# Performance work log

Hardware: AMD Instinct MI355X
Metric: run time of the kernel (lower is better)

Reference implementation:

```python
import jax, jax.numpy as jnp
import numpy as np

N, E = 4096, 131072
IN, HID, OUT = 128, 128, 256
H4, C4 = 4, HID            # first/middle GAT: 4 heads of 128 -> concat 512
CAT = H4 * C4              # 512
NH, DK = 8, OUT // 8       # dense MHA
EPS_LN = 1e-5


def setup_inputs() -> dict:
    key = jax.random.key(0)
    ks = jax.random.split(key, 32)
    s = 0.05
    inp = {
        "x": jax.random.normal(ks[0], (N, IN), jnp.float32),
        "edge_index": jax.random.randint(ks[1], (2, E), 0, N, jnp.int64),
        # GAT layer 0: in=128, heads=4, out=128
        "W0": jax.random.normal(ks[2], (IN, H4 * C4)) * s,
        "as0": jax.random.normal(ks[3], (H4, C4)) * s,
        "ad0": jax.random.normal(ks[4], (H4, C4)) * s,
        "b0": jnp.zeros((H4 * C4,)),
        # GAT layer 1: in=512, heads=4, out=128
        "W1": jax.random.normal(ks[5], (CAT, H4 * C4)) * s,
        "as1": jax.random.normal(ks[6], (H4, C4)) * s,
        "ad1": jax.random.normal(ks[7], (H4, C4)) * s,
        "b1": jnp.zeros((H4 * C4,)),
        # GAT layer 2: in=512, heads=1, out=256
        "W2": jax.random.normal(ks[8], (CAT, OUT)) * s,
        "as2": jax.random.normal(ks[9], (1, OUT)) * s,
        "ad2": jax.random.normal(ks[10], (1, OUT)) * s,
        "b2": jnp.zeros((OUT,)),
        # LayerNorms
        "g0": jnp.ones((CAT,)), "be0": jnp.zeros((CAT,)),
        "g1": jnp.ones((CAT,)), "be1": jnp.zeros((CAT,)),
        "g2": jnp.ones((OUT,)), "be2": jnp.zeros((OUT,)),
        # dense MHA on output_dim=256
        "wq": jax.random.normal(ks[11], (OUT, OUT)) * s, "bq": jnp.zeros((OUT,)),
        "wk": jax.random.normal(ks[12], (OUT, OUT)) * s, "bk": jnp.zeros((OUT,)),
        "wv": jax.random.normal(ks[13], (OUT, OUT)) * s, "bv": jnp.zeros((OUT,)),
        "wo": jax.random.normal(ks[14], (OUT, OUT)) * s, "bo": jnp.zeros((OUT,)),
    }
    return inp


def _layer_norm(x, g, b):
    mu = x.mean(-1, keepdims=True)
    var = ((x - mu) ** 2).mean(-1, keepdims=True)
    return (x - mu) * jax.lax.rsqrt(var + EPS_LN) * g + b


def _gat(x, src, dst, W, a_src, a_dst, bias, heads, out_c):
    # PyG GATConv (concat=True, negative_slope=0.2, self-loops pre-added)
    n = x.shape[0]
    xl = (x @ W).reshape(n, heads, out_c)            # [N,H,C]
    al_s = (xl * a_src).sum(-1)                      # [N,H]
    al_d = (xl * a_dst).sum(-1)                      # [N,H]
    alpha = jax.nn.leaky_relu(al_s[src] + al_d[dst], 0.2)  # [Etot,H]
    m = jax.ops.segment_max(alpha, dst, num_segments=n)
    e = jnp.exp(alpha - m[dst])
    denom = jax.ops.segment_sum(e, dst, num_segments=n)
    w = e / (denom[dst] + 1e-16)                     # [Etot,H]
    msg = w[:, :, None] * xl[src]                    # [Etot,H,C]
    out = jax.ops.segment_sum(msg, dst, num_segments=n)
    return out.reshape(n, heads * out_c) + bias


def _mha(x, wq, bq, wk, bk, wv, bv, wo, bo):
    # x: [1,N,D], 8 heads
    B, S, D = x.shape
    def split(y):
        return y.reshape(B, S, NH, DK).transpose(0, 2, 1, 3)
    Q, K, V = split(x @ wq + bq), split(x @ wk + bk), split(x @ wv + bv)
    scores = jnp.einsum('bhqd,bhkd->bhqk', Q, K) / np.sqrt(DK)
    attn = jax.nn.softmax(scores, axis=-1)
    out = jnp.einsum('bhqk,bhkd->bhqd', attn, V)
    out = out.transpose(0, 2, 1, 3).reshape(B, S, D)
    return out @ wo + bo


def reference(x, edge_index, W0, as0, ad0, b0, W1, as1, ad1, b1, W2, as2, ad2, b2,
              g0, be0, g1, be1, g2, be2, wq, bq, wk, bk, wv, bv, wo, bo):
    n = x.shape[0]
    loops = jnp.arange(n, dtype=edge_index.dtype)
    src = jnp.concatenate([edge_index[0], loops])
    dst = jnp.concatenate([edge_index[1], loops])

    # layer 0: in=128 -> 512; residual None (128 != 512)
    h = jax.nn.elu(_gat(x, src, dst, W0, as0, ad0, b0, H4, C4))
    h = _layer_norm(h, g0, be0)

    # layer 1: 512 -> 512; residual applies
    res = h
    h = jax.nn.elu(_gat(h, src, dst, W1, as1, ad1, b1, H4, C4))
    h = _layer_norm(h, g1, be1)
    h = h + res

    # layer 2: 512 -> 256, 1 head
    h = _gat(h, src, dst, W2, as2, ad2, b2, 1, OUT)
    h = _layer_norm(h, g2, be2)

    # dense self-attention over all nodes as one sequence
    h = _mha(h[None], wq, bq, wk, bk, wv, bv, wo, bo)[0]
    return h
```

## Files before the change

### kernel.cpp

```cpp
#include <hip/hip_runtime.h>
#include <math.h>

typedef __attribute__((ext_vector_type(8))) short short8;
typedef __attribute__((ext_vector_type(4))) float float4v;

#define QS 0.2550354f

#if __has_builtin(__builtin_amdgcn_exp2f)
#define EXP2(x) __builtin_amdgcn_exp2f(x)
#else
#define EXP2(x) __expf((x)*0.6931471805599453f)
#endif

__device__ __forceinline__ float waveReduceSum(float v){
  #pragma unroll
  for(int o=32;o>0;o>>=1) v += __shfl_down(v,o,64);
  return v;
}

__device__ __forceinline__ unsigned short f2bf(float f){
  unsigned int u = __float_as_uint(f);
  return (unsigned short)((u + 0x7FFFu + ((u>>16)&1u)) >> 16);
}
__device__ __forceinline__ float bf2f(unsigned short u){
  return __uint_as_float(((unsigned int)u)<<16);
}

__global__ __launch_bounds__(256) void prep(const float* __restrict__ x, unsigned short* __restrict__ xb,
                     const float* __restrict__ W0, unsigned short* __restrict__ W0t,
                     const float* __restrict__ W1, unsigned short* __restrict__ W1t,
                     const float* __restrict__ W2, unsigned short* __restrict__ W2t,
                     const float* __restrict__ wq, const float* __restrict__ wk,
                     const float* __restrict__ wv, unsigned short* __restrict__ wqkvt,
                     const float* __restrict__ bq, const float* __restrict__ bk,
                     const float* __restrict__ bv, float* __restrict__ bqkv,
                     const float* __restrict__ wo, unsigned short* __restrict__ wot,
                     const float* __restrict__ as0, const float* __restrict__ ad0, unsigned short* __restrict__ S0,
                     const float* __restrict__ as1, const float* __restrict__ ad1, unsigned short* __restrict__ S1,
                     const float* __restrict__ as2, const float* __restrict__ ad2, unsigned short* __restrict__ S2,
                     const int* __restrict__ ei, int E, int Etot, int* __restrict__ hist){
  int b = blockIdx.x, t = threadIdx.x;
  if(b < 256){
    int i = (b*256 + t)*8;
    float4 u0 = *(const float4*)(x + i);
    float4 u1 = *(const float4*)(x + i + 4);
    short8 o;
    o[0]=(short)f2bf(u0.x); o[1]=(short)f2bf(u0.y); o[2]=(short)f2bf(u0.z); o[3]=(short)f2bf(u0.w);
    o[4]=(short)f2bf(u1.x); o[5]=(short)f2bf(u1.y); o[6]=(short)f2bf(u1.z); o[7]=(short)f2bf(u1.w);
    *(short8*)(xb + i) = o;
    return;
  }
  if(b == 256){ bqkv[t] = bq[t]*QS; bqkv[256+t] = bk[t]; bqkv[512+t] = bv[t]; return; }
  if(b < 433){
    __shared__ unsigned short tile[64][65];
    int tb = b - 257;
    const float* src; unsigned short* dst; int K,N,roff,local; float sc = 1.f;
    if(tb<16){src=W0;dst=W0t;K=128;N=512;local=tb;roff=0;}
    else if(tb<80){src=W1;dst=W1t;K=512;N=512;local=tb-16;roff=0;}
    else if(tb<112){src=W2;dst=W2t;K=512;N=256;local=tb-80;roff=0;}
    else if(tb<128){src=wq;dst=wqkvt;K=256;N=256;local=tb-112;roff=0;sc=QS;}
    else if(tb<144){src=wk;dst=wqkvt;K=256;N=256;local=tb-128;roff=256;}
    else if(tb<160){src=wv;dst=wqkvt;K=256;N=256;local=tb-144;roff=512;}
    else {src=wo;dst=wot;K=256;N=256;local=tb-160;roff=0;}
    int ntiles = N>>6;
    int k0 = (local/ntiles)*64, n0 = (local%ntiles)*64;
    int r4 = t>>4, c4 = (t&15)*4;
    #pragma unroll
    for(int it=0;it<4;it++){
      int row = r4 + it*16;
      float4 v = *(const float4*)(src + (size_t)(k0+row)*N + n0 + c4);
      tile[row][c4+0]=f2bf(v.x*sc);
      tile[row][c4+1]=f2bf(v.y*sc);
      tile[row][c4+2]=f2bf(v.z*sc);
      tile[row][c4+3]=f2bf(v.w*sc);
    }
    __syncthreads();
    int r8 = t>>3, c8 = (t&7)*8;
    #pragma unroll
    for(int it=0;it<2;it++){
      int n = r8 + it*32;
      short8 o;
      #pragma unroll
      for(int j=0;j<8;j++) o[j] = (short)tile[c8+j][n];
      *(short8*)(dst + (size_t)(n0+n+roff)*K + k0 + c8) = o;
    }
    return;
  }
  if(b >= 1585){
    int e = (b-1585)*256 + t;
    if(e < Etot){
      int d = (e<E) ? (ei[E+e]&4095) : (e-E);
      atomicAdd(&hist[d], 1);
    }
    return;
  }
  int bb = b - 433;
  const float *W,*as,*ad; unsigned short* S; int K,C,H,k;
  if(bb<128){W=W0;as=as0;ad=ad0;S=S0;K=128;C=128;H=4;k=bb;}
  else if(bb<640){W=W1;as=as1;ad=ad1;S=S1;K=512;C=128;H=4;k=bb-128;}
  else {W=W2;as=as2;ad=ad2;S=S2;K=512;C=256;H=1;k=bb-640;}
  int D = H*C;
  __shared__ float s1[4], s2[4];
  int lane=t&63, wid=t>>6;
  for(int h=0;h<H;h++){
    float ps=0.f, pd=0.f;
    for(int c=t;c<C;c+=256){
      float wv2 = W[k*D + h*C + c];
      ps += wv2*as[h*C+c];
      pd += wv2*ad[h*C+c];
    }
    ps = waveReduceSum(ps); pd = waveReduceSum(pd);
    if(lane==0){ s1[wid]=ps; s2[wid]=pd; }
    __syncthreads();
    if(t==0){
      float u=s1[0]+s1[1]+s1[2]+s1[3], v=s2[0]+s2[1]+s2[2]+s2[3];
      S[h*K+k]=f2bf(u); S[(4+h)*K+k]=f2bf(v);
    }
    __syncthreads();
  }
  if(t==0){
    for(int h=H;h<4;h++){ S[h*K+k]=0; S[(4+h)*K+k]=0; }
    for(int r=8;r<16;r++) S[r*K+k]=0;
  }
}

__global__ __launch_bounds__(256) void gemm_mfma(const unsigned short* __restrict__ A,
                                                 const unsigned short* __restrict__ Bt,
                                                 const float* __restrict__ bias,
                                                 float* __restrict__ C,
                                                 unsigned short* __restrict__ Cb,
                                                 unsigned short* __restrict__ VtT,
                                                 const unsigned short* __restrict__ Wsd,
                                                 float* __restrict__ als,
                                                 float* __restrict__ ald,
                                                 int M, int K, int N){
  int t = threadIdx.x, lane = t & 63, w = t >> 6;
  int m = lane & 15, g = lane >> 4;
  int bm = blockIdx.y * 64, bn = blockIdx.x * 64;

  __shared__ unsigned short As[2][64*72];
  __shared__ unsigned short Bs[2][64*72];

  int sr = t >> 3;
  int sc = (t & 7) * 8;
  const unsigned short* Ap = A  + (bm + sr)*K + sc;
  const unsigned short* Bp = Bt + (bn + sr)*K + sc;
  bool doC = (Wsd != nullptr) && (blockIdx.x == 0);

  float4v acc[4];
  #pragma unroll
  for(int nt=0;nt<4;nt++) acc[nt] = (float4v){0.f,0.f,0.f,0.f};
  float4v acc2 = (float4v){0.f,0.f,0.f,0.f};

  short8 a0 = *(const short8*)(Ap);
  short8 a1 = *(const short8*)(Ap + 32*K);
  short8 b0 = *(const short8*)(Bp);
  short8 b1 = *(const short8*)(Bp + 32*K);

  int buf = 0;
  for(int k0=0;k0<K;k0+=64){
    *(short8*)&As[buf][sr*72 + sc]      = a0;
    *(short8*)&As[buf][(sr+32)*72 + sc] = a1;
    *(short8*)&Bs[buf][sr*72 + sc]      = b0;
    *(short8*)&Bs[buf][(sr+32)*72 + sc] = b1;
    if(k0+64 < K){
      a0 = *(const short8*)(Ap + k0+64);
      a1 = *(const short8*)(Ap + 32*K + k0+64);
      b0 = *(const short8*)(Bp + k0+64);
      b1 = *(const short8*)(Bp + 32*K + k0+64);
    }
    __syncthreads();

    #pragma unroll
    for(int ks=0;ks<2;ks++){
      short8 aA = *(const short8*)&As[buf][(w*16 + m)*72 + ks*32 + g*8];
      #pragma unroll
      for(int nt=0;nt<4;nt++){
        short8 bB = *(const short8*)&Bs[buf][(nt*16 + m)*72 + ks*32 + g*8];
        acc[nt] = __builtin_amdgcn_mfma_f32_16x16x32_bf16(aA, bB, acc[nt], 0,0,0);
      }
      if(doC){
        short8 bW = *(const short8*)(Wsd + m*K + k0 + ks*32 + g*8);
        acc2 = __builtin_amdgcn_mfma_f32_16x16x32_bf16(aA, bW, acc2, 0,0,0);
      }
    }
    buf ^= 1;
  }

  if(VtT && bn >= 512){
    __syncthreads();
    unsigned short* T = &As[0][0];
    #pragma unroll
    for(int nt=0;nt<4;nt++){
      int col = bn + nt*16 + m;
      float bv = bias ? bias[col] : 0.f;
      unsigned int r0 = __float_as_uint(acc[nt][0]+bv) + 0x8000u;
      unsigned int r1 = __float_as_uint(acc[nt][1]+bv) + 0x8000u;
      unsigned int r2 = __float_as_uint(acc[nt][2]+bv) + 0x8000u;
      unsigned int r3 = __float_as_uint(acc[nt][3]+bv) + 0x8000u;
      uint2 pk;
      pk.x = __builtin_amdgcn_perm(r1, r0, 0x07060302u);
      pk.y = __builtin_amdgcn_perm(r3, r2, 0x07060302u);
      *(uint2*)&T[(nt*16 + m)*72 + w*16 + g*4] = pk;
    }
    __syncthreads();
    int d  = t >> 2;
    int qc = (t & 3) * 16;
    short8 v0 = *(const short8*)&T[d*72 + qc];
    short8 v1 = *(const short8*)&T[d*72 + qc + 8];
    unsigned short* dst = VtT + (size_t)(bn - 512 + d)*M + bm + qc;
    *(short8*)(dst)     = v0;
    *(short8*)(dst + 8) = v1;
    return;
  }

  #pragma unroll
  for(int nt=0;nt<4;nt++){
    int col = bn + nt*16 + m;
    float bv = bias ? bias[col] : 0.f;
    #pragma unroll
    for(int r=0;r<4;r++){
      int row = bm + w*16 + g*4 + r;
      float v = acc[nt][r] + bv;
      if(C)  C[row*N + col]  = v;
      if(Cb) Cb[row*N + col] = f2bf(v);
    }
  }
  if(doC){
    #pragma unroll
    for(int r=0;r<4;r++){
      int row = bm + w*16 + g*4 + r;
      if(m<4)      als[row*4 + m]     = acc2[r];
      else if(m<8) ald[row*4 + (m-4)] = acc2[r];
    }
  }
}

__global__ __launch_bounds__(1024) void csr_scan(const int* __restrict__ hist,
                                                 int* __restrict__ row_ptr,
                                                 int* __restrict__ wcnt, int N){
  __shared__ int sh[1024];
  int t = threadIdx.x;
  int base[4];
  int s = 0;
  #pragma unroll
  for(int i=0;i<4;i++){ base[i]=s; s += hist[t*4+i]; }
  sh[t] = s;
  __syncthreads();
  for(int off=1; off<1024; off<<=1){
    int x = (t>=off) ? sh[t-off] : 0;
    __syncthreads();
    sh[t] += x;
    __syncthreads();
  }
  int excl = (t==0) ? 0 : sh[t-1];
  #pragma unroll
  for(int i=0;i<4;i++){
    row_ptr[t*4+i] = excl + base[i];
    wcnt[t*4+i]    = excl + base[i];
  }
  if(t==1023) row_ptr[N] = excl + s;
}

__global__ void csr_scatter(const int* __restrict__ ei, int E, int Etot,
                            int* __restrict__ wcnt, int* __restrict__ col){
  int e = blockIdx.x*256 + threadIdx.x;
  if(e>=Etot) return;
  int s,d;
  if(e<E){ s=ei[e]&4095; d=ei[E+e]&4095; } else { s=d=e-E; }
  int pos = atomicAdd(&wcnt[d], 1);
  col[pos] = s;
}

#define CE 128
__global__ void gat_gather_ln(const int* __restrict__ rp,
                              const int* __restrict__ col,
                              const unsigned short* __restrict__ xlb,
                              const float* __restrict__ als,
                              const float* __restrict__ ald,
                              const float* __restrict__ bias,
                              const float* __restrict__ gw,
                              const float* __restrict__ be,
                              const float* __restrict__ res,
                              float* __restrict__ out,
                              unsigned short* __restrict__ outb,
                              int D, int logC, int do_elu){
  int n = blockIdx.x, t = threadIdx.x;
  int c0 = t*2;
  int h = c0 >> logC;
  int rowW = D >> 1;
  float4 advv = *(const float4*)(ald + n*4);
  int start = rp[n], end = rp[n+1];
  const unsigned int* xw = (const unsigned int*)xlb;

  __shared__ float pw[2][CE*4];
  __shared__ int offs[2][CE];

  float acc0=0.f, acc1=0.f, den=0.f;
  int nch = (end - start + CE - 1) / CE;

  {
    int cnt = min(CE, end-start);
    if(t < cnt){
      int s = col[start+t];
      offs[0][t] = s*rowW;
      float4 av = *(const float4*)(als + s*4);
      #pragma unroll
      for(int hh=0;hh<4;hh++){
        float a = ((const float*)&av)[hh] + ((const float*)&advv)[hh];
        a = a>0.f ? a : 0.2f*a;
        pw[0][t*4+hh] = __expf(a);
      }
    }
  }

  for(int c=0;c<nch;c++){
    __syncthreads();
    if(c+1 < nch){
      int base = start + (c+1)*CE;
      int cnt = min(CE, end-base);
      int b2 = (c+1)&1;
      if(t < cnt){
        int s = col[base+t];
        offs[b2][t] = s*rowW;
        float4 av = *(const float4*)(als + s*4);
        #pragma unroll
        for(int hh=0;hh<4;hh++){
          float a = ((const float*)&av)[hh] + ((const float*)&advv)[hh];
          a = a>0.f ? a : 0.2f*a;
          pw[b2][t*4+hh] = __expf(a);
        }
      }
    }
    int base = start + c*CE;
    int cnt = min(CE, end-base);
    int b = c&1;
    #pragma unroll 8
    for(int j=0;j<cnt;j++){
      float p = pw[b][j*4+h];
      unsigned int u = xw[offs[b][j] + t];
      acc0 += p * bf2f((unsigned short)(u & 0xffffu));
      acc1 += p * bf2f((unsigned short)(u >> 16));
      den += p;
    }
  }

  float inv_d = 1.f/(den + 1e-16f);
  float v0 = acc0*inv_d + bias[c0];
  float v1 = acc1*inv_d + bias[c0+1];
  if(do_elu){
    v0 = v0>0.f ? v0 : expm1f(v0);
    v1 = v1>0.f ? v1 : expm1f(v1);
  }
  __shared__ float sh[4];
  int lane=t&63, wid=t>>6, nw = blockDim.x>>6;
  float sum = waveReduceSum(v0+v1);
  if(lane==0) sh[wid]=sum;
  __syncthreads();
  float mean = 0.f;
  for(int i=0;i<nw;i++) mean += sh[i];
  mean /= (float)D;
  __syncthreads();
  float d0 = v0-mean, d1 = v1-mean;
  float vs = waveReduceSum(d0*d0 + d1*d1);
  if(lane==0) sh[wid]=vs;
  __syncthreads();
  float var = 0.f;
  for(int i=0;i<nw;i++) var += sh[i];
  var /= (float)D;
  float inv = rsqrtf(var + 1e-5f);
  float y0 = d0*inv*gw[c0]   + be[c0];
  float y1 = d1*inv*gw[c0+1] + be[c0+1];
  if(res){ float2 rv = *(const float2*)(res + n*D + c0); y0 += rv.x; y1 += rv.y; }
  if(out) *(float2*)(out + n*D + c0) = make_float2(y0, y1);
  if(outb) ((unsigned int*)outb)[n*rowW + t] =
      (unsigned int)f2bf(y0) | ((unsigned int)f2bf(y1) << 16);
}

#define KS 4
__global__ __launch_bounds__(256) void attention12(const unsigned short* __restrict__ QKV,
                                                   const unsigned short* __restrict__ Vt,
                                                   float* __restrict__ Op,
                                                   float* __restrict__ lp, int S){
  const int RS = 768;
  int qb = blockIdx.x * 64;
  int h  = blockIdx.y;
  int ks = blockIdx.z;
  int t  = threadIdx.x;
  int lane = t & 63, w = t >> 6;
  int m = lane & 15, g = lane >> 4;
  int m7 = m & 7;

  __shared__ unsigned short Ps[64*64];
  __shared__ unsigned short Vs[32*64];
  __shared__ unsigned short Ks[64*36];

  short8 aQ = *(const short8*)(QKV + (qb + w*16 + m)*RS + h*32 + g*8);

  float4v o0 = {0.f,0.f,0.f,0.f}, o1 = {0.f,0.f,0.f,0.f};
  float den = 0.f;

  int r8 = t>>3, c8 = t&7;
  int kr = t>>2, kc = (t&3)*8;
  int kA = ks*(S/KS), kB = kA + S/KS;

  short8 v  = *(const short8*)(Vt + (h*32 + r8)*S + kA + c8*8);
  short8 kv = *(const short8*)(QKV + (kA + kr)*RS + 256 + h*32 + kc);

  for(int kt=kA; kt<kB; kt+=64){
    __syncthreads();
    *(short8*)&Vs[r8*64 + ((c8 ^ (r8&7))<<3)] = v;
    *(short8*)&Ks[kr*36 + kc] = kv;
    if(kt+64 < kB){
      v  = *(const short8*)(Vt + (h*32 + r8)*S + kt+64 + c8*8);
      kv = *(const short8*)(QKV + (kt+64 + kr)*RS + 256 + h*32 + kc);
    }
    __syncthreads();

    #pragma unroll
    for(int nt=0;nt<4;nt++){
      short8 aK = *(const short8*)&Ks[(nt*16 + m)*36 + g*8];
      float4v acc = {0.f,0.f,0.f,0.f};
      acc = __builtin_amdgcn_mfma_f32_16x16x32_bf16(aK, aQ, acc, 0,0,0);
      float p0 = EXP2(acc[0]);
      float p1 = EXP2(acc[1]);
      float p2 = EXP2(acc[2]);
      float p3 = EXP2(acc[3]);
      den += (p0+p1)+(p2+p3);
      unsigned int r0 = __float_as_uint(p0) + 0x8000u;
      unsigned int r1 = __float_as_uint(p1) + 0x8000u;
      unsigned int r2 = __float_as_uint(p2) + 0x8000u;
      unsigned int r3 = __float_as_uint(p3) + 0x8000u;
      uint2 pk;
      pk.x = __builtin_amdgcn_perm(r1, r0, 0x07060302u);
      pk.y = __builtin_amdgcn_perm(r3, r2, 0x07060302u);
      *(uint2*)&Ps[(w*16 + m)*64 + (((2*nt + (g>>1)) ^ m7)<<3) + ((g&1)<<2)] = pk;
    }

    #pragma unroll
    for(int kh=0;kh<2;kh++){
      int swz = ((kh*4 + g) ^ m7) << 3;
      short8 aP  = *(const short8*)&Ps[(w*16 + m)*64 + swz];
      short8 bV0 = *(const short8*)&Vs[m*64       + swz];
      short8 bV1 = *(const short8*)&Vs[(16+m)*64  + swz];
      o0 = __builtin_amdgcn_mfma_f32_16x16x32_bf16(aP, bV0, o0, 0,0,0);
      o1 = __builtin_amdgcn_mfma_f32_16x16x32_bf16(aP, bV1, o1, 0,0,0);
    }
  }

  den += __shfl_xor(den, 16, 64);
  den += __shfl_xor(den, 32, 64);

  float* Ob = Op + (size_t)ks*S*256;
  #pragma unroll
  for(int r=0;r<4;r++){
    int q = qb + w*16 + g*4 + r;
    Ob[q*256 + h*32 + m]      = o0[r];
    Ob[q*256 + h*32 + 16 + m] = o1[r];
  }
  if(g==0){
    int q = qb + w*16 + m;
    lp[ks*S*8 + q*8 + h] = den;
  }
}

__global__ __launch_bounds__(256) void combine(const float* __restrict__ Op,
                                               const float* __restrict__ lp,
                                               unsigned short* __restrict__ aob, int S){
  int q = blockIdx.x, t = threadIdx.x;
  int h = t >> 5;
  float o = 0.f, l = 0.f;
  #pragma unroll
  for(int s=0;s<KS;s++) o += Op[(size_t)s*S*256 + q*256 + t];
  #pragma unroll
  for(int s=0;s<KS;s++) l += lp[s*S*8 + q*8 + h];
  aob[q*256 + t] = f2bf(o / l);
}

extern "C" void kernel_launch(void* const* d_in, const int* in_sizes, int n_in,
                              void* d_out, int out_size, void* d_ws, size_t ws_size,
                              hipStream_t stream) {
  const float* x   = (const float*)d_in[0];
  const int*   ei  = (const int*)d_in[1];
  const float* W0  = (const float*)d_in[2];
  const float* as0 = (const float*)d_in[3];
  const float* ad0 = (const float*)d_in[4];
  const float* b0  = (const float*)d_in[5];
  const float* W1  = (const float*)d_in[6];
  const float* as1 = (const float*)d_in[7];
  const float* ad1 = (const float*)d_in[8];
  const float* b1  = (const float*)d_in[9];
  const float* W2  = (const float*)d_in[10];
  const float* as2 = (const float*)d_in[11];
  const float* ad2 = (const float*)d_in[12];
  const float* b2  = (const float*)d_in[13];
  const float* g0  = (const float*)d_in[14];
  const float* be0 = (const float*)d_in[15];
  const float* g1  = (const float*)d_in[16];
  const float* be1 = (const float*)d_in[17];
  const float* g2  = (const float*)d_in[18];
  const float* be2 = (const float*)d_in[19];
  const float* wq  = (const float*)d_in[20];
  const float* bq  = (const float*)d_in[21];
  const float* wk  = (const float*)d_in[22];
  const float* bk  = (const float*)d_in[23];
  const float* wv  = (const float*)d_in[24];
  const float* bv  = (const float*)d_in[25];
  const float* wo  = (const float*)d_in[26];
  const float* bo  = (const float*)d_in[27];
  float* out = (float*)d_out;

  const int N = 4096;
  const int E = in_sizes[1] / 2;
  const int Etot = E + N;

  char* p = (char*)d_ws;
  auto alloc = [&](size_t bytes){ char* r = p; p += (bytes + 255) & ~(size_t)255; return r; };

  float* h0   = (float*)alloc(N*512*4);
  float* als  = (float*)alloc(N*4*4);
  float* ald  = (float*)alloc(N*4*4);
  unsigned short* xb   = (unsigned short*)alloc(N*128*2);
  unsigned short* xlb  = (unsigned short*)alloc(N*512*2);
  unsigned short* h0b  = (unsigned short*)alloc(N*512*2);
  unsigned short* h1b  = (unsigned short*)alloc(N*512*2);
  unsigned short* h2b  = (unsigned short*)alloc(N*256*2);
  unsigned short* QKVb = (unsigned short*)alloc((size_t)N*768*2);
  unsigned short* Vt   = (unsigned short*)alloc(256*N*2);
  unsigned short* aob  = (unsigned short*)alloc(N*256*2);
  unsigned short* W0t  = (unsigned short*)alloc(512*128*2);
  unsigned short* W1t  = (unsigned short*)alloc(512*512*2);
  unsigned short* W2t  = (unsigned short*)alloc(256*512*2);
  unsigned short* wqkvt= (unsigned short*)alloc(768*256*2);
  float* bqkv = (float*)alloc(768*4);
  unsigned short* wot  = (unsigned short*)alloc(256*256*2);
  unsigned short* Wsd0 = (unsigned short*)alloc(16*128*2);
  unsigned short* Wsd1 = (unsigned short*)alloc(16*512*2);
  unsigned short* Wsd2 = (unsigned short*)alloc(16*512*2);
  float* Op = (float*)alloc((size_t)KS*N*256*4);
  float* lp = (float*)alloc((size_t)KS*N*8*4);
  int* hist = (int*)alloc(N*4);
  int* wcnt = (int*)alloc(N*4);
  int* rp   = (int*)alloc((N+2)*4);
  int* col  = (int*)alloc(Etot*4);

  hipMemsetAsync(hist, 0, N*sizeof(int), stream);
  prep<<<1585 + (Etot+255)/256, 256, 0, stream>>>(x, xb, W0, W0t, W1, W1t, W2, W2t,
                                 wq, wk, wv, wqkvt, bq, bk, bv, bqkv, wo, wot,
                                 as0, ad0, Wsd0, as1, ad1, Wsd1, as2, ad2, Wsd2,
                                 ei, E, Etot, hist);

  csr_scan<<<1, 1024, 0, stream>>>(hist, rp, wcnt, N);
  csr_scatter<<<(Etot+255)/256, 256, 0, stream>>>(ei, E, Etot, wcnt, col);

  gemm_mfma<<<dim3(8, 64), 256, 0, stream>>>(xb, W0t, nullptr, nullptr, xlb, nullptr, Wsd0, als, ald, N, 128, 512);
  gat_gather_ln<<<N, 256, 0, stream>>>(rp, col, xlb, als, ald, b0, g0, be0,
                                       nullptr, h0, h0b, 512, 7, 1);

  gemm_mfma<<<dim3(8, 64), 256, 0, stream>>>(h0b, W1t, nullptr, nullptr, xlb, nullptr, Wsd1, als, ald, N, 512, 512);
  gat_gather_ln<<<N, 256, 0, stream>>>(rp, col, xlb, als, ald, b1, g1, be1,
                                       h0, nullptr, h1b, 512, 7, 1);

  gemm_mfma<<<dim3(4, 64), 256, 0, stream>>>(h1b, W2t, nullptr, nullptr, xlb, nullptr, Wsd2, als, ald, N, 512, 256);
  gat_gather_ln<<<N, 128, 0, stream>>>(rp, col, xlb, als, ald, b2, g2, be2,
                                       nullptr, nullptr, h2b, 256, 8, 0);

  gemm_mfma<<<dim3(12, 64), 256, 0, stream>>>(h2b, wqkvt, bqkv, nullptr, QKVb, Vt, nullptr, nullptr, nullptr, N, 256, 768);
  attention12<<<dim3(N/64, 8, KS), 256, 0, stream>>>(QKVb, Vt, Op, lp, N);
  combine<<<N, 256, 0, stream>>>(Op, lp, aob, N);
  gemm_mfma<<<dim3(4, 64), 256, 0, stream>>>(aob, wot, bo, out, nullptr, nullptr, nullptr, nullptr, nullptr, N, 256, 256);
}
```

Before: 268.1 us.

## Fuse whole pipeline into one cooperative persistent kernel with grid syncs

Replaces the sequence of separate launches (prep, CSR scan/scatter, GEMMs, GAT gathers, attention, combine, output GEMM) with a single cooperative megakernel of 512 persistent blocks that loop over work units and separate stages with grid.sync(). It aims to remove per-launch overhead and the inter-kernel gaps between about fourteen small kernels. The attention path appears restructured into a per-block unit writing aob directly, dropping the split-K partial buffers and combine pass. In exchange, each stage is limited to 512 blocks with shared-memory reuse, occupancy is capped, and grid-wide barriers add their own latency.

Result: slower. 1.029 ms (+283.9%).

```diff
diff --git a/kernel.cpp b/kernel.cpp
--- a/kernel.cpp
+++ b/kernel.cpp
@@ -1,10 +1,14 @@
 #include <hip/hip_runtime.h>
+#include <hip/hip_cooperative_groups.h>
 #include <math.h>
+
+namespace cg = cooperative_groups;
 
 typedef __attribute__((ext_vector_type(8))) short short8;
 typedef __attribute__((ext_vector_type(4))) float float4v;
 
 #define QS 0.2550354f
+#define NB 512
 
 #if __has_builtin(__builtin_amdgcn_exp2f)
 #define EXP2(x) __builtin_amdgcn_exp2f(x)
@@ -17,7 +21,6 @@
   for(int o=32;o>0;o>>=1) v += __shfl_down(v,o,64);
   return v;
 }
-
 __device__ __forceinline__ unsigned short f2bf(float f){
   unsigned int u = __float_as_uint(f);
   return (unsigned short)((u + 0x7FFFu + ((u>>16)&1u)) >> 16);
@@ -26,81 +29,65 @@
   return __uint_as_float(((unsigned int)u)<<16);
 }
 
-__global__ __launch_bounds__(256) void prep(const float* __restrict__ x, unsigned short* __restrict__ xb,
-                     const float* __restrict__ W0, unsigned short* __restrict__ W0t,
-                     const float* __restrict__ W1, unsigned short* __restrict__ W1t,
-                     const float* __restrict__ W2, unsigned short* __restrict__ W2t,
-                     const float* __restrict__ wq, const float* __restrict__ wk,
-                     const float* __restrict__ wv, unsigned short* __restrict__ wqkvt,
-                     const float* __restrict__ bq, const float* __restrict__ bk,
-                     const float* __restrict__ bv, float* __restrict__ bqkv,
-                     const float* __restrict__ wo, unsigned short* __restrict__ wot,
-                     const float* __restrict__ as0, const float* __restrict__ ad0, unsigned short* __restrict__ S0,
-                     const float* __restrict__ as1, const float* __restrict__ ad1, unsigned short* __restrict__ S1,
-                     const float* __restrict__ as2, const float* __restrict__ ad2, unsigned short* __restrict__ S2,
-                     const int* __restrict__ ei, int E, int Etot, int* __restrict__ hist){
-  int b = blockIdx.x, t = threadIdx.x;
-  if(b < 256){
-    int i = (b*256 + t)*8;
-    float4 u0 = *(const float4*)(x + i);
-    float4 u1 = *(const float4*)(x + i + 4);
+struct MP {
+  const float* x; const int* ei;
+  const float *W0,*as0,*ad0,*b0;
+  const float *W1,*as1,*ad1,*b1;
+  const float *W2,*as2,*ad2,*b2;
+  const float *g0,*be0,*g1,*be1,*g2,*be2;
+  const float *wq,*bq,*wk,*bk,*wv,*bv,*wo,*bo;
+  float* out;
+  float *h0,*als,*ald,*bqkv;
+  unsigned short *xb,*xlb,*h0b,*h1b,*h2b,*QKVb,*Vt,*aob;
+  unsigned short *W0t,*W1t,*W2t,*wqkvt,*wot,*Wsd0,*Wsd1,*Wsd2;
+  int *hist,*wcnt,*rp,*col;
+  int E, Etot;
+};
+
+
+__device__ void transpose_unit(int tb, const MP& P, char* smem){
+  int t = threadIdx.x;
+  unsigned short (*tile)[65] = (unsigned short(*)[65])smem;
+  const float* src; unsigned short* dst; int K,N,roff,local; float sc = 1.f;
+  if(tb<16){src=P.W0;dst=P.W0t;K=128;N=512;local=tb;roff=0;}
+  else if(tb<80){src=P.W1;dst=P.W1t;K=512;N=512;local=tb-16;roff=0;}
+  else if(tb<112){src=P.W2;dst=P.W2t;K=512;N=256;local=tb-80;roff=0;}
+  else if(tb<128){src=P.wq;dst=P.wqkvt;K=256;N=256;local=tb-112;roff=0;sc=QS;}
+  else if(tb<144){src=P.wk;dst=P.wqkvt;K=256;N=256;local=tb-128;roff=256;}
+  else if(tb<160){src=P.wv;dst=P.wqkvt;K=256;N=256;local=tb-144;roff=512;}
+  else {src=P.wo;dst=P.wot;K=256;N=256;local=tb-160;roff=0;}
+  int ntiles = N>>6;
+  int k0 = (local/ntiles)*64, n0 = (local%ntiles)*64;
+  int r4 = t>>4, c4 = (t&15)*4;
+  #pragma unroll
+  for(int it=0;it<4;it++){
+    int row = r4 + it*16;
+    float4 v = *(const float4*)(src + (size_t)(k0+row)*N + n0 + c4);
+    tile[row][c4+0]=f2bf(v.x*sc);
+    tile[row][c4+1]=f2bf(v.y*sc);
+    tile[row][c4+2]=f2bf(v.z*sc);
+    tile[row][c4+3]=f2bf(v.w*sc);
+  }
+  __syncthreads();
+  int r8 = t>>3, c8 = (t&7)*8;
+  #pragma unroll
+  for(int it=0;it<2;it++){
+    int n = r8 + it*32;
     short8 o;
-    o[0]=(short)f2bf(u0.x); o[1]=(short)f2bf(u0.y); o[2]=(short)f2bf(u0.z); o[3]=(short)f2bf(u0.w);
-    o[4]=(short)f2bf(u1.x); o[5]=(short)f2bf(u1.y); o[6]=(short)f2bf(u1.z); o[7]=(short)f2bf(u1.w);
-    *(short8*)(xb + i) = o;
-    return;
-  }
-  if(b == 256){ bqkv[t] = bq[t]*QS; bqkv[256+t] = bk[t]; bqkv[512+t] = bv[t]; return; }
-  if(b < 433){
-    __shared__ unsigned short tile[64][65];
-    int tb = b - 257;
-    const float* src; unsigned short* dst; int K,N,roff,local; float sc = 1.f;
-    if(tb<16){src=W0;dst=W0t;K=128;N=512;local=tb;roff=0;}
-    else if(tb<80){src=W1;dst=W1t;K=512;N=512;local=tb-16;roff=0;}
-    else if(tb<112){src=W2;dst=W2t;K=512;N=256;local=tb-80;roff=0;}
-    else if(tb<128){src=wq;dst=wqkvt;K=256;N=256;local=tb-112;roff=0;sc=QS;}
-    else if(tb<144){src=wk;dst=wqkvt;K=256;N=256;local=tb-128;roff=256;}
-    else if(tb<160){src=wv;dst=wqkvt;K=256;N=256;local=tb-144;roff=512;}
-    else {src=wo;dst=wot;K=256;N=256;local=tb-160;roff=0;}
-    int ntiles = N>>6;
-    int k0 = (local/ntiles)*64, n0 = (local%ntiles)*64;
-    int r4 = t>>4, c4 = (t&15)*4;
     #pragma unroll
-    for(int it=0;it<4;it++){
-      int row = r4 + it*16;
-      float4 v = *(const float4*)(src + (size_t)(k0+row)*N + n0 + c4);
-      tile[row][c4+0]=f2bf(v.x*sc);
-      tile[row][c4+1]=f2bf(v.y*sc);
-      tile[row][c4+2]=f2bf(v.z*sc);
-      tile[row][c4+3]=f2bf(v.w*sc);
-    }
-    __syncthreads();
-    int r8 = t>>3, c8 = (t&7)*8;
-    #pragma unroll
-    for(int it=0;it<2;it++){
-      int n = r8 + it*32;
-      short8 o;
-      #pragma unroll
-      for(int j=0;j<8;j++) o[j] = (short)tile[c8+j][n];
-      *(short8*)(dst + (size_t)(n0+n+roff)*K + k0 + c8) = o;
-    }
-    return;
-  }
-  if(b >= 1585){
-    int e = (b-1585)*256 + t;
-    if(e < Etot){
-      int d = (e<E) ? (ei[E+e]&4095) : (e-E);
-      atomicAdd(&hist[d], 1);
-    }
-    return;
-  }
-  int bb = b - 433;
+    for(int j=0;j<8;j++) o[j] = (short)tile[c8+j][n];
+    *(short8*)(dst + (size_t)(n0+n+roff)*K + k0 + c8) = o;
+  }
+}
+
+__device__ void wsd_unit(int bb, const MP& P, char* smem){
+  int t = threadIdx.x;
+  float* s1 = (float*)smem; float* s2 = s1+4;
   const float *W,*as,*ad; unsigned short* S; int K,C,H,k;
-  if(bb<128){W=W0;as=as0;ad=ad0;S=S0;K=128;C=128;H=4;k=bb;}
-  else if(bb<640){W=W1;as=as1;ad=ad1;S=S1;K=512;C=128;H=4;k=bb-128;}
-  else {W=W2;as=as2;ad=ad2;S=S2;K=512;C=256;H=1;k=bb-640;}
+  if(bb<128){W=P.W0;as=P.as0;ad=P.ad0;S=P.Wsd0;K=128;C=128;H=4;k=bb;}
+  else if(bb<640){W=P.W1;as=P.as1;ad=P.ad1;S=P.Wsd1;K=512;C=128;H=4;k=bb-128;}
+  else {W=P.W2;as=P.as2;ad=P.ad2;S=P.Wsd2;K=512;C=256;H=1;k=bb-640;}
   int D = H*C;
-  __shared__ float s1[4], s2[4];
   int lane=t&63, wid=t>>6;
   for(int h=0;h<H;h++){
     float ps=0.f, pd=0.f;
@@ -124,28 +111,48 @@
   }
 }
 
-__global__ __launch_bounds__(256) void gemm_mfma(const unsigned short* __restrict__ A,
-                                                 const unsigned short* __restrict__ Bt,
-                                                 const float* __restrict__ bias,
-                                                 float* __restrict__ C,
-                                                 unsigned short* __restrict__ Cb,
-                                                 unsigned short* __restrict__ VtT,
-                                                 const unsigned short* __restrict__ Wsd,
-                                                 float* __restrict__ als,
-                                                 float* __restrict__ ald,
-                                                 int M, int K, int N){
+__device__ void scan_block(const int* __restrict__ hist, int* __restrict__ rp,
+                           int* __restrict__ wcnt, char* smem){
+  int t = threadIdx.x;
+  int* sh = (int*)smem;
+  int loc[16]; int s=0;
+  #pragma unroll
+  for(int i=0;i<16;i++){ loc[i]=s; s += hist[t*16+i]; }
+  sh[t] = s;
+  __syncthreads();
+  for(int off=1; off<256; off<<=1){
+    int x = (t>=off) ? sh[t-off] : 0;
+    __syncthreads();
+    sh[t] += x;
+    __syncthreads();
+  }
+  int excl = (t==0) ? 0 : sh[t-1];
+  #pragma unroll
+  for(int i=0;i<16;i++){
+    int v = excl + loc[i];
+    rp[t*16+i] = v; wcnt[t*16+i] = v;
+  }
+  if(t==255) rp[4096] = excl + s;
+}
+
+__device__ void gemm_unit(int u, int nbx,
+                          const unsigned short* __restrict__ A, const unsigned short* __restrict__ Bt,
+                          const float* __restrict__ bias, float* __restrict__ C,
+                          unsigned short* __restrict__ Cb, unsigned short* __restrict__ VtT,
+                          const unsigned short* __restrict__ Wsd, float* __restrict__ als,
+                          float* __restrict__ ald, int M, int K, int N, char* smem){
   int t = threadIdx.x, lane = t & 63, w = t >> 6;
   int m = lane & 15, g = lane >> 4;
-  int bm = blockIdx.y * 64, bn = blockIdx.x * 64;
-
-  __shared__ unsigned short As[2][64*72];
-  __shared__ unsigned short Bs[2][64*72];
+  int bx = u % nbx, by = u / nbx;
+  int bm = by * 64, bn = bx * 64;
+  unsigned short* As = (unsigned short*)smem;
+  unsigned short* Bs = (unsigned short*)(smem + 18432);
 
   int sr = t >> 3;
   int sc = (t & 7) * 8;
-  const unsigned short* Ap = A  + (bm + sr)*K + sc;
-  const unsigned short* Bp = Bt + (bn + sr)*K + sc;
-  bool doC = (Wsd != nullptr) && (blockIdx.x == 0);
+  const unsigned short* Ap = A  + (size_t)(bm + sr)*K + sc;
+  const unsigned short* Bp = Bt + (size_t)(bn + sr)*K + sc;
+  bool doC = (Wsd != nullptr) && (bx == 0);
 
   float4v acc[4];
   #pragma unroll
@@ -159,10 +166,10 @@
 
   int buf = 0;
   for(int k0=0;k0<K;k0+=64){
-    *(short8*)&As[buf][sr*72 + sc]      = a0;
-    *(short8*)&As[buf][(sr+32)*72 + sc] = a1;
-    *(short8*)&Bs[buf][sr*72 + sc]      = b0;
-    *(short8*)&Bs[buf][(sr+32)*72 + sc] = b1;
+    *(short8*)&As[buf*4608 + sr*72 + sc]      = a0;
+    *(short8*)&As[buf*4608 + (sr+32)*72 + sc] = a1;
+    *(short8*)&Bs[buf*4608 + sr*72 + sc]      = b0;
+    *(short8*)&Bs[buf*4608 + (sr+32)*72 + sc] = b1;
     if(k0+64 < K){
       a0 = *(const short8*)(Ap + k0+64);
       a1 = *(const short8*)(Ap + 32*K + k0+64);
@@ -173,10 +180,10 @@
 
     #pragma unroll
     for(int ks=0;ks<2;ks++){
-      short8 aA = *(const short8*)&As[buf][(w*16 + m)*72 + ks*32 + g*8];
+      short8 aA = *(const short8*)&As[buf*4608 + (w*16 + m)*72 + ks*32 + g*8];
       #pragma unroll
       for(int nt=0;nt<4;nt++){
-        short8 bB = *(const short8*)&Bs[buf][(nt*16 + m)*72 + ks*32 + g*8];
+        short8 bB = *(const short8*)&Bs[buf*4608 + (nt*16 + m)*72 + ks*32 + g*8];
         acc[nt] = __builtin_amdgcn_mfma_f32_16x16x32_bf16(aA, bB, acc[nt], 0,0,0);
       }
       if(doC){
@@ -187,9 +194,9 @@
     buf ^= 1;
   }
 
-  if(VtT && bn >= 512){
-    __syncthreads();
-    unsigned short* T = &As[0][0];
+  if(VtT != nullptr && bn >= 512){
+    __syncthreads();
+    unsigned short* T = As;
     #pragma unroll
     for(int nt=0;nt<4;nt++){
       int col = bn + nt*16 + m;
@@ -211,90 +218,50 @@
     unsigned short* dst = VtT + (size_t)(bn - 512 + d)*M + bm + qc;
     *(short8*)(dst)     = v0;
     *(short8*)(dst + 8) = v1;
-    return;
-  }
-
-  #pragma unroll
-  for(int nt=0;nt<4;nt++){
-    int col = bn + nt*16 + m;
-    float bv = bias ? bias[col] : 0.f;
+  } else {
     #pragma unroll
-    for(int r=0;r<4;r++){
-      int row = bm + w*16 + g*4 + r;
-      float v = acc[nt][r] + bv;
-      if(C)  C[row*N + col]  = v;
-      if(Cb) Cb[row*N + col] = f2bf(v);
-    }
-  }
-  if(doC){
-    #pragma unroll
-    for(int r=0;r<4;r++){
-      int row = bm + w*16 + g*4 + r;
-      if(m<4)      als[row*4 + m]     = acc2[r];
-      else if(m<8) ald[row*4 + (m-4)] = acc2[r];
-    }
-  }
-}
-
-__global__ __launch_bounds__(1024) void csr_scan(const int* __restrict__ hist,
-                                                 int* __restrict__ row_ptr,
-                                                 int* __restrict__ wcnt, int N){
-  __shared__ int sh[1024];
+    for(int nt=0;nt<4;nt++){
+      int col = bn + nt*16 + m;
+      float bv = bias ? bias[col] : 0.f;
+      #pragma unroll
+      for(int r=0;r<4;r++){
+        int row = bm + w*16 + g*4 + r;
+        float v = acc[nt][r] + bv;
+        if(C)  C[(size_t)row*N + col]  = v;
+        if(Cb) Cb[(size_t)row*N + col] = f2bf(v);
+      }
+    }
+    if(doC){
+      #pragma unroll
+      for(int r=0;r<4;r++){
+        int row = bm + w*16 + g*4 + r;
+        if(m<4)      als[row*4 + m]     = acc2[r];
+        else if(m<8) ald[row*4 + (m-4)] = acc2[r];
+      }
+    }
+  }
+  __syncthreads();
+}
+
+#define CE 128
+__device__ void gat_node(int n, const int* __restrict__ rp, const int* __restrict__ col,
+                         const unsigned short* __restrict__ xlb,
+                         const float* __restrict__ als, const float* __restrict__ ald,
+                         const float* __restrict__ bias, const float* __restrict__ gw,
+                         const float* __restrict__ be, const float* __restrict__ res,
+                         float* __restrict__ out, unsigned short* __restrict__ outb,
+                         int D, int logC, int do_elu, int nw, char* smem){
   int t = threadIdx.x;
-  int base[4];
-  int s = 0;
-  #pragma unroll
-  for(int i=0;i<4;i++){ base[i]=s; s += hist[t*4+i]; }
-  sh[t] = s;
-  __syncthreads();
-  for(int off=1; off<1024; off<<=1){
-    int x = (t>=off) ? sh[t-off] : 0;
-    __syncthreads();
-    sh[t] += x;
-    __syncthreads();
-  }
-  int excl = (t==0) ? 0 : sh[t-1];
-  #pragma unroll
-  for(int i=0;i<4;i++){
-    row_ptr[t*4+i] = excl + base[i];
-    wcnt[t*4+i]    = excl + base[i];
-  }
-  if(t==1023) row_ptr[N] = excl + s;
-}
-
-__global__ void csr_scatter(const int* __restrict__ ei, int E, int Etot,
-                            int* __restrict__ wcnt, int* __restrict__ col){
-  int e = blockIdx.x*256 + threadIdx.x;
-  if(e>=Etot) return;
-  int s,d;
-  if(e<E){ s=ei[e]&4095; d=ei[E+e]&4095; } else { s=d=e-E; }
-  int pos = atomicAdd(&wcnt[d], 1);
-  col[pos] = s;
-}
-
-#define CE 128
-__global__ void gat_gather_ln(const int* __restrict__ rp,
-                              const int* __restrict__ col,
-                              const unsigned short* __restrict__ xlb,
-                              const float* __restrict__ als,
-                              const float* __restrict__ ald,
-                              const float* __restrict__ bias,
-                              const float* __restrict__ gw,
-                              const float* __restrict__ be,
-                              const float* __restrict__ res,
-                              float* __restrict__ out,
-                              unsigned short* __restrict__ outb,
-                              int D, int logC, int do_elu){
-  int n = blockIdx.x, t = threadIdx.x;
+  float* pw  = (float*)smem;
+  int*  offs = (int*)(smem + 4096);
+  float* shv = (float*)(smem + 4096 + 1024);
+  int halfD = D >> 1;
+  bool act = t < halfD;
   int c0 = t*2;
   int h = c0 >> logC;
-  int rowW = D >> 1;
   float4 advv = *(const float4*)(ald + n*4);
   int start = rp[n], end = rp[n+1];
   const unsigned int* xw = (const unsigned int*)xlb;
-
-  __shared__ float pw[2][CE*4];
-  __shared__ int offs[2][CE];
 
   float acc0=0.f, acc1=0.f, den=0.f;
   int nch = (end - start + CE - 1) / CE;
@@ -303,13 +270,13 @@
     int cnt = min(CE, end-start);
     if(t < cnt){
       int s = col[start+t];
-      offs[0][t] = s*rowW;
+      offs[t] = s*halfD;
       float4 av = *(const float4*)(als + s*4);
       #pragma unroll
       for(int hh=0;hh<4;hh++){
         float a = ((const float*)&av)[hh] + ((const float*)&advv)[hh];
         a = a>0.f ? a : 0.2f*a;
-        pw[0][t*4+hh] = __expf(a);
+        pw[t*4+hh] = __expf(a);
       }
     }
   }
@@ -317,18 +284,18 @@
   for(int c=0;c<nch;c++){
     __syncthreads();
     if(c+1 < nch){
-      int base = start + (c+1)*CE;
-      int cnt = min(CE, end-base);
+      int base2 = start + (c+1)*CE;
+      int cnt = min(CE, end-base2);
       int b2 = (c+1)&1;
       if(t < cnt){
-        int s = col[base+t];
-        offs[b2][t] = s*rowW;
+        int s = col[base2+t];
+        offs[b2*CE+t] = s*halfD;
         float4 av = *(const float4*)(als + s*4);
         #pragma unroll
         for(int hh=0;hh<4;hh++){
           float a = ((const float*)&av)[hh] + ((const float*)&advv)[hh];
           a = a>0.f ? a : 0.2f*a;
-          pw[b2][t*4+hh] = __expf(a);
+          pw[b2*CE*4 + t*4+hh] = __expf(a);
         }
       }
     }
@@ -337,83 +304,84 @@
     int b = c&1;
     #pragma unroll 8
     for(int j=0;j<cnt;j++){
-      float p = pw[b][j*4+h];
-      unsigned int u = xw[offs[b][j] + t];
+      float p = pw[b*CE*4 + j*4+h];
+      unsigned int u = xw[offs[b*CE+j] + t];
       acc0 += p * bf2f((unsigned short)(u & 0xffffu));
       acc1 += p * bf2f((unsigned short)(u >> 16));
       den += p;
     }
   }
 
-  float inv_d = 1.f/(den + 1e-16f);
-  float v0 = acc0*inv_d + bias[c0];
-  float v1 = acc1*inv_d + bias[c0+1];
-  if(do_elu){
-    v0 = v0>0.f ? v0 : expm1f(v0);
-    v1 = v1>0.f ? v1 : expm1f(v1);
-  }
-  __shared__ float sh[4];
-  int lane=t&63, wid=t>>6, nw = blockDim.x>>6;
+  float v0=0.f, v1=0.f;
+  if(act){
+    float inv_d = 1.f/(den + 1e-16f);
+    v0 = acc0*inv_d + bias[c0];
+    v1 = acc1*inv_d + bias[c0+1];
+    if(do_elu){
+      v0 = v0>0.f ? v0 : expm1f(v0);
+      v1 = v1>0.f ? v1 : expm1f(v1);
+    }
+  }
+  int lane=t&63, wid=t>>6;
   float sum = waveReduceSum(v0+v1);
-  if(lane==0) sh[wid]=sum;
+  if(lane==0) shv[wid]=sum;
   __syncthreads();
   float mean = 0.f;
-  for(int i=0;i<nw;i++) mean += sh[i];
+  for(int i=0;i<nw;i++) mean += shv[i];
   mean /= (float)D;
   __syncthreads();
-  float d0 = v0-mean, d1 = v1-mean;
+  float d0 = act ? v0-mean : 0.f;
+  float d1 = act ? v1-mean : 0.f;
   float vs = waveReduceSum(d0*d0 + d1*d1);
-  if(lane==0) sh[wid]=vs;
+  if(lane==0) shv[wid]=vs;
   __syncthreads();
   float var = 0.f;
-  for(int i=0;i<nw;i++) var += sh[i];
+  for(int i=0;i<nw;i++) var += shv[i];
   var /= (float)D;
   float inv = rsqrtf(var + 1e-5f);
-  float y0 = d0*inv*gw[c0]   + be[c0];
-  float y1 = d1*inv*gw[c0+1] + be[c0+1];
-  if(res){ float2 rv = *(const float2*)(res + n*D + c0); y0 += rv.x; y1 += rv.y; }
-  if(out) *(float2*)(out + n*D + c0) = make_float2(y0, y1);
-  if(outb) ((unsigned int*)outb)[n*rowW + t] =
-      (unsigned int)f2bf(y0) | ((unsigned int)f2bf(y1) << 16);
-}
-
-#define KS 4
-__global__ __launch_bounds__(256) void attention12(const unsigned short* __restrict__ QKV,
-                                                   const unsigned short* __restrict__ Vt,
-                                                   float* __restrict__ Op,
-                                                   float* __restrict__ lp, int S){
+  if(act){
+    float y0 = d0*inv*gw[c0]   + be[c0];
+    float y1 = d1*inv*gw[c0+1] + be[c0+1];
+    if(res){ float2 rv = *(const float2*)(res + (size_t)n*D + c0); y0 += rv.x; y1 += rv.y; }
+    if(out) *(float2*)(out + (size_t)n*D + c0) = make_float2(y0, y1);
+    if(outb) ((unsigned int*)outb)[(size_t)n*halfD + t] =
+        (unsigned int)f2bf(y0) | ((unsigned int)f2bf(y1) << 16);
+  }
+}
+
+__device__ void attn_unit(int u, const unsigned short* __restrict__ QKV,
+                          const unsigned short* __restrict__ Vt,
+                          unsigned short* __restrict__ aob, int S, char* smem){
   const int RS = 768;
-  int qb = blockIdx.x * 64;
-  int h  = blockIdx.y;
-  int ks = blockIdx.z;
+  int qb = (u >> 3) * 64;
+  int h  = u & 7;
   int t  = threadIdx.x;
   int lane = t & 63, w = t >> 6;
   int m = lane & 15, g = lane >> 4;
   int m7 = m & 7;
 
-  __shared__ unsigned short Ps[64*64];
-  __shared__ unsigned short Vs[32*64];
-  __shared__ unsigned short Ks[64*36];
-
-  short8 aQ = *(const short8*)(QKV + (qb + w*16 + m)*RS + h*32 + g*8);
+  unsigned short* Ps = (unsigned short*)smem;
+  unsigned short* Vs = (unsigned short*)(smem + 8192);
+  unsigned short* Ks = (unsigned short*)(smem + 12288);
+
+  short8 aQ = *(const short8*)(QKV + (size_t)(qb + w*16 + m)*RS + h*32 + g*8);
 
   float4v o0 = {0.f,0.f,0.f,0.f}, o1 = {0.f,0.f,0.f,0.f};
   float den = 0.f;
 
   int r8 = t>>3, c8 = t&7;
   int kr = t>>2, kc = (t&3)*8;
-  int kA = ks*(S/KS), kB = kA + S/KS;
-
-  short8 v  = *(const short8*)(Vt + (h*32 + r8)*S + kA + c8*8);
-  short8 kv = *(const short8*)(QKV + (kA + kr)*RS + 256 + h*32 + kc);
-
-  for(int kt=kA; kt<kB; kt+=64){
+
+  short8 v  = *(const short8*)(Vt + (size_t)(h*32 + r8)*S + c8*8);
+  short8 kv = *(const short8*)(QKV + (size_t)kr*RS + 256 + h*32 + kc);
+
+  for(int kt=0; kt<S; kt+=64){
     __syncthreads();
     *(short8*)&Vs[r8*64 + ((c8 ^ (r8&7))<<3)] = v;
     *(short8*)&Ks[kr*36 + kc] = kv;
-    if(kt+64 < kB){
-      v  = *(const short8*)(Vt + (h*32 + r8)*S + kt+64 + c8*8);
-      kv = *(const short8*)(QKV + (kt+64 + kr)*RS + 256 + h*32 + kc);
+    if(kt+64 < S){
+      v  = *(const short8*)(Vt + (size_t)(h*32 + r8)*S + kt+64 + c8*8);
+      kv = *(const short8*)(QKV + (size_t)(kt+64 + kr)*RS + 256 + h*32 + kc);
     }
     __syncthreads();
 
@@ -451,65 +419,111 @@
   den += __shfl_xor(den, 16, 64);
   den += __shfl_xor(den, 32, 64);
 
-  float* Ob = Op + (size_t)ks*S*256;
   #pragma unroll
   for(int r=0;r<4;r++){
+    float dd = __shfl(den, g*4 + r, 64);
     int q = qb + w*16 + g*4 + r;
-    Ob[q*256 + h*32 + m]      = o0[r];
-    Ob[q*256 + h*32 + 16 + m] = o1[r];
-  }
-  if(g==0){
-    int q = qb + w*16 + m;
-    lp[ks*S*8 + q*8 + h] = den;
-  }
-}
-
-__global__ __launch_bounds__(256) void combine(const float* __restrict__ Op,
-                                               const float* __restrict__ lp,
-                                               unsigned short* __restrict__ aob, int S){
-  int q = blockIdx.x, t = threadIdx.x;
-  int h = t >> 5;
-  float o = 0.f, l = 0.f;
-  #pragma unroll
-  for(int s=0;s<KS;s++) o += Op[(size_t)s*S*256 + q*256 + t];
-  #pragma unroll
-  for(int s=0;s<KS;s++) l += lp[s*S*8 + q*8 + h];
-  aob[q*256 + t] = f2bf(o / l);
+    aob[(size_t)q*256 + h*32 + m]      = f2bf(o0[r]/dd);
+    aob[(size_t)q*256 + h*32 + 16 + m] = f2bf(o1[r]/dd);
+  }
+}
+
+__global__ __launch_bounds__(256, 2) void mega(MP P){
+  __shared__ __attribute__((aligned(16))) char smem[36880];
+  cg::grid_group grid = cg::this_grid();
+  int blk = blockIdx.x, t = threadIdx.x;
+
+  { int gid = blk*256 + t; if(gid < 4096) P.hist[gid] = 0; }
+  for(int u=blk; u<1585; u+=NB){
+    if(u < 256){
+      int i = (u*256 + t)*8;
+      float4 u0 = *(const float4*)(P.x + i);
+      float4 u1 = *(const float4*)(P.x + i + 4);
+      short8 o;
+      o[0]=(short)f2bf(u0.x); o[1]=(short)f2bf(u0.y); o[2]=(short)f2bf(u0.z); o[3]=(short)f2bf(u0.w);
+      o[4]=(short)f2bf(u1.x); o[5]=(short)f2bf(u1.y); o[6]=(short)f2bf(u1.z); o[7]=(short)f2bf(u1.w);
+      *(short8*)(P.xb + i) = o;
+    } else if(u == 256){
+      P.bqkv[t] = P.bq[t]*QS; P.bqkv[256+t] = P.bk[t]; P.bqkv[512+t] = P.bv[t];
+    } else if(u < 433){
+      transpose_unit(u-257, P, smem);
+    } else {
+      wsd_unit(u-433, P, smem);
+    }
+    __syncthreads();
+  }
+  grid.sync();
+
+  for(int u=blk; u<528; u+=NB){
+    int e = u*256 + t;
+    if(e < P.Etot){
+      int d = (e < P.E) ? (P.ei[P.E+e] & 4095) : (e - P.E);
+      atomicAdd(&P.hist[d], 1);
+    }
+  }
+  grid.sync();
+
+  if(blk == 0) scan_block(P.hist, P.rp, P.wcnt, smem);
+  grid.sync();
+
+  for(int u=blk; u<1040; u+=NB){
+    if(u < 512){
+      gemm_unit(u, 8, P.xb, P.W0t, nullptr, nullptr, P.xlb, nullptr,
+                P.Wsd0, P.als, P.ald, 4096, 128, 512, smem);
+    } else {
+      int e = (u-512)*256 + t;
+      if(e < P.Etot){
+        int s,d;
+        if(e < P.E){ s = P.ei[e]&4095; d = P.ei[P.E+e]&4095; } else { s = d = e - P.E; }
+        int pos = atomicAdd(&P.wcnt[d], 1);
+        P.col[pos] = s;
+      }
+      __syncthreads();
+    }
+  }
+  grid.sync();
+
+  for(int n=blk; n<4096; n+=NB)
+    gat_node(n, P.rp, P.col, P.xlb, P.als, P.ald, P.b0, P.g0, P.be0,
+             nullptr, P.h0, P.h0b, 512, 7, 1, 4, smem);
+  grid.sync();
+
+  for(int u=blk; u<512; u+=NB)
+    gemm_unit(u, 8, P.h0b, P.W1t, nullptr, nullptr, P.xlb, nullptr,
+              P.Wsd1, P.als, P.ald, 4096, 512, 512, smem);
+  grid.sync();
+
+  for(int n=blk; n<4096; n+=NB)
+    gat_node(n, P.rp, P.col, P.xlb, P.als, P.ald, P.b1, P.g1, P.be1,
+             P.h0, nullptr, P.h1b, 512, 7, 1, 4, smem);
+  grid.sync();
+
+  for(int u=blk; u<256; u+=NB)
+    gemm_unit(u, 4, P.h1b, P.W2t, nullptr, nullptr, P.xlb, nullptr,
+              P.Wsd2, P.als, P.ald, 4096, 512, 256, smem);
+  grid.sync();
+
+  for(int n=blk; n<4096; n+=NB)
+    gat_node(n, P.rp, P.col, P.xlb, P.als, P.ald, P.b2, P.g2, P.be2,
+             nullptr, nullptr, P.h2b, 256, 8, 0, 2, smem);
+  grid.sync();
+
+  for(int u=blk; u<768; u+=NB)
+    gemm_unit(u, 12, P.h2b, P.wqkvt, P.bqkv, nullptr, P.QKVb, P.Vt,
+              nullptr, nullptr, nullptr, 4096, 256, 768, smem);
+  grid.sync();
+
+  attn_unit(blk, P.QKVb, P.Vt, P.aob, 4096, smem);
+  grid.sync();
+
+  for(int u=blk; u<256; u+=NB)
+    gemm_unit(u, 4, P.aob, P.wot, P.bo, P.out, nullptr, nullptr,
+              nullptr, nullptr, nullptr, 4096, 256, 256, smem);
 }
 
 extern "C" void kernel_launch(void* const* d_in, const int* in_sizes, int n_in,
                               void* d_out, int out_size, void* d_ws, size_t ws_size,
                               hipStream_t stream) {
-  const float* x   = (const float*)d_in[0];
-  const int*   ei  = (const int*)d_in[1];
-  const float* W0  = (const float*)d_in[2];
-  const float* as0 = (const float*)d_in[3];
-  const float* ad0 = (const float*)d_in[4];
-  const float* b0  = (const float*)d_in[5];
-  const float* W1  = (const float*)d_in[6];
-  const float* as1 = (const float*)d_in[7];
-  const float* ad1 = (const float*)d_in[8];
-  const float* b1  = (const float*)d_in[9];
-  const float* W2  = (const float*)d_in[10];
-  const float* as2 = (const float*)d_in[11];
-  const float* ad2 = (const float*)d_in[12];
-  const float* b2  = (const float*)d_in[13];
-  const float* g0  = (const float*)d_in[14];
-  const float* be0 = (const float*)d_in[15];
-  const float* g1  = (const float*)d_in[16];
-  const float* be1 = (const float*)d_in[17];
-  const float* g2  = (const float*)d_in[18];
-  const float* be2 = (const float*)d_in[19];
-  const float* wq  = (const float*)d_in[20];
-  const float* bq  = (const float*)d_in[21];
-  const float* wk  = (const float*)d_in[22];
-  const float* bk  = (const float*)d_in[23];
-  const float* wv  = (const float*)d_in[24];
-  const float* bv  = (const float*)d_in[25];
-  const float* wo  = (const float*)d_in[26];
-  const float* bo  = (const float*)d_in[27];
-  float* out = (float*)d_out;
-
   const int N = 4096;
   const int E = in_sizes[1] / 2;
   const int Etot = E + N;
@@ -517,56 +531,63 @@
   char* p = (char*)d_ws;
   auto alloc = [&](size_t bytes){ char* r = p; p += (bytes + 255) & ~(size_t)255; return r; };
 
-  float* h0   = (float*)alloc(N*512*4);
-  float* als  = (float*)alloc(N*4*4);
-  float* ald  = (float*)alloc(N*4*4);
-  unsigned short* xb   = (unsigned short*)alloc(N*128*2);
-  unsigned short* xlb  = (unsigned short*)alloc(N*512*2);
-  unsigned short* h0b  = (unsigned short*)alloc(N*512*2);
-  unsigned short* h1b  = (unsigned short*)alloc(N*512*2);
-  unsigned short* h2b  = (unsigned short*)alloc(N*256*2);
-  unsigned short* QKVb = (unsigned short*)alloc((size_t)N*768*2);
-  unsigned short* Vt   = (unsigned short*)alloc(256*N*2);
-  unsigned short* aob  = (unsigned short*)alloc(N*256*2);
-  unsigned short* W0t  = (unsigned short*)alloc(512*128*2);
-  unsigned short* W1t  = (unsigned short*)alloc(512*512*2);
-  unsigned short* W2t  = (unsigned short*)alloc(256*512*2);
-  unsigned short* wqkvt= (unsigned short*)alloc(768*256*2);
-  float* bqkv = (float*)alloc(768*4);
-  unsigned short* wot  = (unsigned short*)alloc(256*256*2);
-  unsigned short* Wsd0 = (unsigned short*)alloc(16*128*2);
-  unsigned short* Wsd1 = (unsigned short*)alloc(16*512*2);
-  unsigned short* Wsd2 = (unsigned short*)alloc(16*512*2);
-  float* Op = (float*)alloc((size_t)KS*N*256*4);
-  float* lp = (float*)alloc((size_t)KS*N*8*4);
-  int* hist = (int*)alloc(N*4);
-  int* wcnt = (int*)alloc(N*4);
-  int* rp   = (int*)alloc((N+2)*4);
-  int* col  = (int*)alloc(Etot*4);
-
-  hipMemsetAsync(hist, 0, N*sizeof(int), stream);
-  prep<<<1585 + (Etot+255)/256, 256, 0, stream>>>(x, xb, W0, W0t, W1, W1t, W2, W2t,
-                                 wq, wk, wv, wqkvt, bq, bk, bv, bqkv, wo, wot,
-                                 as0, ad0, Wsd0, as1, ad1, Wsd1, as2, ad2, Wsd2,
-                                 ei, E, Etot, hist);
-
-  csr_scan<<<1, 1024, 0, stream>>>(hist, rp, wcnt, N);
-  csr_scatter<<<(Etot+255)/256, 256, 0, stream>>>(ei, E, Etot, wcnt, col);
-
-  gemm_mfma<<<dim3(8, 64), 256, 0, stream>>>(xb, W0t, nullptr, nullptr, xlb, nullptr, Wsd0, als, ald, N, 128, 512);
-  gat_gather_ln<<<N, 256, 0, stream>>>(rp, col, xlb, als, ald, b0, g0, be0,
-                                       nullptr, h0, h0b, 512, 7, 1);
-
-  gemm_mfma<<<dim3(8, 64), 256, 0, stream>>>(h0b, W1t, nullptr, nullptr, xlb, nullptr, Wsd1, als, ald, N, 512, 512);
-  gat_gather_ln<<<N, 256, 0, stream>>>(rp, col, xlb, als, ald, b1, g1, be1,
-                                       h0, nullptr, h1b, 512, 7, 1);
-
-  gemm_mfma<<<dim3(4, 64), 256, 0, stream>>>(h1b, W2t, nullptr, nullptr, xlb, nullptr, Wsd2, als, ald, N, 512, 256);
-  gat_gather_ln<<<N, 128, 0, stream>>>(rp, col, xlb, als, ald, b2, g2, be2,
-                                       nullptr, nullptr, h2b, 256, 8, 0);
-
-  gemm_mfma<<<dim3(12, 64), 256, 0, stream>>>(h2b, wqkvt, bqkv, nullptr, QKVb, Vt, nullptr, nullptr, nullptr, N, 256, 768);
-  attention12<<<dim3(N/64, 8, KS), 256, 0, stream>>>(QKVb, Vt, Op, lp, N);
-  combine<<<N, 256, 0, stream>>>(Op, lp, aob, N);
-  gemm_mfma<<<dim3(4, 64), 256, 0, stream>>>(aob, wot, bo, out, nullptr, nullptr, nullptr, nullptr, nullptr, N, 256, 256);
-}
+  MP P;
+  P.x   = (const float*)d_in[0];
+  P.ei  = (const int*)d_in[1];
+  P.W0  = (const float*)d_in[2];
+  P.as0 = (const float*)d_in[3];
+  P.ad0 = (const float*)d_in[4];
+  P.b0  = (const float*)d_in[5];
+  P.W1  = (const float*)d_in[6];
+  P.as1 = (const float*)d_in[7];
+  P.ad1 = (const float*)d_in[8];
+  P.b1  = (const float*)d_in[9];
+  P.W2  = (const float*)d_in[10];
+  P.as2 = (const float*)d_in[11];
+  P.ad2 = (const float*)d_in[12];
+  P.b2  = (const float*)d_in[13];
+  P.g0  = (const float*)d_in[14];
+  P.be0 = (const float*)d_in[15];
+  P.g1  = (const float*)d_in[16];
+  P.be1 = (const float*)d_in[17];
+  P.g2  = (const float*)d_in[18];
+  P.be2 = (const float*)d_in[19];
+  P.wq  = (const float*)d_in[20];
+  P.bq  = (const float*)d_in[21];
+  P.wk  = (const float*)d_in[22];
+  P.bk  = (const float*)d_in[23];
+  P.wv  = (const float*)d_in[24];
+  P.bv  = (const float*)d_in[25];
+  P.wo  = (const float*)d_in[26];
+  P.bo  = (const float*)d_in[27];
+  P.out = (float*)d_out;
+
+  P.h0   = (float*)alloc((size_t)N*512*4);
+  P.als  = (float*)alloc(N*4*4);
+  P.ald  = (float*)alloc(N*4*4);
+  P.xb   = (unsigned short*)alloc((size_t)N*128*2);
+  P.xlb  = (unsigned short*)alloc((size_t)N*512*2);
+  P.h0b  = (unsigned short*)alloc((size_t)N*512*2);
+  P.h1b  = (unsigned short*)alloc((size_t)N*512*2);
+  P.h2b  = (unsigned short*)alloc((size_t)N*256*2);
+  P.QKVb = (unsigned short*)alloc((size_t)N*768*2);
+  P.Vt   = (unsigned short*)alloc((size_t)256*N*2);
+  P.aob  = (unsigned short*)alloc((size_t)N*256*2);
+  P.W0t  = (unsigned short*)alloc(512*128*2);
+  P.W1t  = (unsigned short*)alloc(512*512*2);
+  P.W2t  = (unsigned short*)alloc(256*512*2);
+  P.wqkvt= (unsigned short*)alloc(768*256*2);
+  P.bqkv = (float*)alloc(768*4);
+  P.wot  = (unsigned short*)alloc(256*256*2);
+  P.Wsd0 = (unsigned short*)alloc(16*128*2);
+  P.Wsd1 = (unsigned short*)alloc(16*512*2);
+  P.Wsd2 = (unsigned short*)alloc(16*512*2);
+  P.hist = (int*)alloc(N*4);
+  P.wcnt = (int*)alloc(N*4);
+  P.rp   = (int*)alloc((N+2)*4);
+  P.col  = (int*)alloc((size_t)Etot*4);
+  P.E = E; P.Etot = Etot;
+
+  void* kargs[] = { (void*)&P };
+  hipLaunchCooperativeKernel((const void*)mega, dim3(NB), dim3(256), kargs, 0, stream);
+}
```
